# Performance work log

Hardware: AMD Instinct MI355X
Metric: run time of the kernel (lower is better)

Reference implementation:

```python
import jax, jax.numpy as jnp
import numpy as np

B, N, T, S = 1, 16, 2048, 2048
G, I = 1, 2
M = N // G  # heads per group


def setup_inputs() -> dict:
    key = jax.random.key(0)
    ks = jax.random.split(key, 8)
    return {
        "inputs": jax.random.normal(ks[0], (B, N, T, S), dtype=jnp.float32),
        "qw1": jax.random.normal(ks[1], (B, T, G, I, M), dtype=jnp.float32) * 0.05,
        "qw2": jax.random.normal(ks[2], (B, T, G, I, M), dtype=jnp.float32) * 0.05,
        "kw1": jax.random.normal(ks[3], (B, S, G, I, M), dtype=jnp.float32) * 0.05,
        "kw2": jax.random.normal(ks[4], (B, S, G, I, M), dtype=jnp.float32) * 0.05,
        "qdd": jax.random.normal(ks[5], (B, T, G, M), dtype=jnp.float32) * 0.05,
        "kdd": jax.random.normal(ks[6], (B, S, G, M), dtype=jnp.float32) * 0.05,
        "w": jax.random.normal(ks[7], (G, M, M), dtype=jnp.float32) * 0.02,
    }


def reference(inputs, qw1, qw2, kw1, kw2, qdd, kdd, w):
    b, n, t, s = inputs.shape
    g, m = w.shape[0], w.shape[1]
    x = inputs.reshape(b, g, m, t, s)  # BGMTS
    # static cross-head mixing (w + identity)
    wi = w + jnp.eye(m, dtype=w.dtype)
    ret = jnp.einsum('BGMTS,GMN->BGNTS', x, wi)
    # dynamic low-rank mixing, query-side (per T position); the original loops
    # over the I axis — summing over I is mathematically identical.
    hq = jnp.einsum('BGMTS,BTGIM->BGITS', x, qw1)
    ret = ret + jnp.einsum('BGITS,BTGIM->BGMTS', hq, qw2)
    # dynamic low-rank mixing, key-side (per S position)
    hk = jnp.einsum('BGMTS,BSGIM->BGITS', x, kw1)
    ret = ret + jnp.einsum('BGITS,BSGIM->BGMTS', hk, kw2)
    # dynamic diagonal terms
    ret = ret + jnp.einsum('BGMTS,BTGM->BGMTS', x, qdd)
    ret = ret + jnp.einsum('BGMTS,BSGM->BGMTS', x, kdd)
    return ret.reshape(b, n, t, s)
```

## Files before the change

kernel.cpp:

```cpp
#include <hip/hip_runtime.h>


#define TDIM 2048
#define SDIM 2048
#define TT 8
#define SBLK 256

typedef float vf4 __attribute__((ext_vector_type(4)));

__global__ void chp_prep(const float* __restrict__ kw1, const float* __restrict__ kw2,
                         const float* __restrict__ kdd,
                         float* __restrict__ kt1, float* __restrict__ kt2,
                         float* __restrict__ kddt) {
  int tid = blockIdx.x * blockDim.x + threadIdx.x;
  if (tid < 65536) {
    int im = tid >> 11, s = tid & 2047;
    kt1[tid] = kw1[s * 32 + im];
  } else if (tid < 131072) {
    int v = tid - 65536;
    int im = v >> 11, s = v & 2047;
    kt2[v] = kw2[s * 32 + im];
  } else if (tid < 163840) {
    int v = tid - 131072;
    int n = v >> 11, s = v & 2047;
    kddt[v] = kdd[s * 16 + n];
  }
}

__device__ __forceinline__ vf4 ld4(const float* p) {
  return *reinterpret_cast<const vf4*>(p);
}
__device__ __forceinline__ void fma4(vf4& d, const vf4& a, const vf4& b) {
  d.x = fmaf(a.x, b.x, d.x); d.y = fmaf(a.y, b.y, d.y);
  d.z = fmaf(a.z, b.z, d.z); d.w = fmaf(a.w, b.w, d.w);
}
__device__ __forceinline__ void fma4s(vf4& d, const vf4& a, float b) {
  d.x = fmaf(a.x, b, d.x); d.y = fmaf(a.y, b, d.y);
  d.z = fmaf(a.z, b, d.z); d.w = fmaf(a.w, b, d.w);
}

template <bool KT>
__global__ __launch_bounds__(256, 3) void chp_main(
    const float* __restrict__ in, const float* __restrict__ w,
    const float* __restrict__ qw1, const float* __restrict__ qw2,
    const float* __restrict__ qdd, const float* __restrict__ kw1,
    const float* __restrict__ kw2, const float* __restrict__ kdd,
    const float* __restrict__ kt1, const float* __restrict__ kt2,
    const float* __restrict__ kddt, float* __restrict__ out) {
  __shared__ vf4 x_lds[2][16][65];
  __shared__ float wq_lds[2][256];

  const int tid = threadIdx.x;
  const int j = tid & 3;
  const int qg = tid >> 2;
  const int s0 = blockIdx.x * SBLK + qg * 4;
  const int t0 = blockIdx.y * TT;

  vf4 kt1v[2][4], kt2v[2][4], kdv[4];
  if constexpr (KT) {
#pragma unroll
    for (int i = 0; i < 2; ++i)
#pragma unroll
      for (int k = 0; k < 4; ++k) {
        kt1v[i][k] = ld4(kt1 + (size_t)(i * 16 + 4 * j + k) * SDIM + s0);
        kt2v[i][k] = ld4(kt2 + (size_t)(i * 16 + 4 * j + k) * SDIM + s0);
      }
#pragma unroll
    for (int k = 0; k < 4; ++k) kdv[k] = ld4(kddt + (size_t)(4 * j + k) * SDIM + s0);
  } else {
#pragma unroll
    for (int i = 0; i < 2; ++i)
#pragma unroll
      for (int k = 0; k < 4; ++k)
#pragma unroll
        for (int c = 0; c < 4; ++c) {
          kt1v[i][k][c] = kw1[(size_t)(s0 + c) * 32 + i * 16 + 4 * j + k];
          kt2v[i][k][c] = kw2[(size_t)(s0 + c) * 32 + i * 16 + 4 * j + k];
        }
#pragma unroll
    for (int k = 0; k < 4; ++k)
#pragma unroll
      for (int c = 0; c < 4; ++c) kdv[k][c] = kdd[(size_t)(s0 + c) * 16 + 4 * j + k];
  }

  const int bm = tid >> 4, bn = tid & 15;
  const float wbase = w[bm * 16 + bn];

  vf4 xp[4];
#pragma unroll
  for (int k = 0; k < 4; ++k)
    xp[k] = ld4(in + ((size_t)(4 * j + k) * TDIM + t0) * SDIM + s0);
  float q1a = qw1[t0 * 32 + bm], q1b = qw1[t0 * 32 + 16 + bm];
  float q2a = qw2[t0 * 32 + bn], q2b = qw2[t0 * 32 + 16 + bn];
  float qd = qdd[t0 * 16 + bn];

#pragma unroll
  for (int k = 0; k < 4; ++k) x_lds[0][4 * j + k][qg] = xp[k];
  {
    float v = fmaf(q1a, q2a, wbase);
    v = fmaf(q1b, q2b, v);
    if (bm == bn) v += 1.0f + qd;
    wq_lds[0][tid] = v;
  }
  {
    const int t1 = t0 + 1;
#pragma unroll
    for (int k = 0; k < 4; ++k)
      xp[k] = ld4(in + ((size_t)(4 * j + k) * TDIM + t1) * SDIM + s0);
    q1a = qw1[t1 * 32 + bm]; q1b = qw1[t1 * 32 + 16 + bm];
    q2a = qw2[t1 * 32 + bn]; q2b = qw2[t1 * 32 + 16 + bn];
    qd = qdd[t1 * 16 + bn];
  }
  __syncthreads();

  int cur = 0;
  for (int tt = 0; tt < TT; ++tt) {
    const int t = t0 + tt;
    const int nxt = cur ^ 1;

    vf4 acc[4];
    vf4 p0 = (vf4){0.f, 0.f, 0.f, 0.f}, p1 = p0;
#pragma unroll
    for (int r = 0; r < 4; ++r) acc[r] = (vf4){0.f, 0.f, 0.f, 0.f};

#pragma unroll
    for (int m = 0; m < 16; ++m) {
      const vf4 xm = x_lds[cur][m][qg];
      const vf4 wr = *reinterpret_cast<const vf4*>(&wq_lds[cur][m * 16 + 4 * j]);
      fma4s(acc[0], xm, wr.x);
      fma4s(acc[1], xm, wr.y);
      fma4s(acc[2], xm, wr.z);
      fma4s(acc[3], xm, wr.w);
      if ((m >> 2) == j) {
        const int k = m & 3;
        fma4(p0, xm, kt1v[0][k]);
        fma4(p1, xm, kt1v[1][k]);
        fma4(acc[k], xm, kdv[k]);
      }
    }
#pragma unroll
    for (int mask = 1; mask <= 2; mask <<= 1) {
      p0.x += __shfl_xor(p0.x, mask); p0.y += __shfl_xor(p0.y, mask);
      p0.z += __shfl_xor(p0.z, mask); p0.w += __shfl_xor(p0.w, mask);
      p1.x += __shfl_xor(p1.x, mask); p1.y += __shfl_xor(p1.y, mask);
      p1.z += __shfl_xor(p1.z, mask); p1.w += __shfl_xor(p1.w, mask);
    }
#pragma unroll
    for (int r = 0; r < 4; ++r) {
      fma4(acc[r], p0, kt2v[0][r]);
      fma4(acc[r], p1, kt2v[1][r]);
      *reinterpret_cast<vf4*>(out + ((size_t)(4 * j + r) * TDIM + t) * SDIM + s0) =
          acc[r];
    }

    if (tt + 1 < TT) {
#pragma unroll
      for (int k = 0; k < 4; ++k) x_lds[nxt][4 * j + k][qg] = xp[k];
      float v = fmaf(q1a, q2a, wbase);
      v = fmaf(q1b, q2b, v);
      if (bm == bn) v += 1.0f + qd;
      wq_lds[nxt][tid] = v;
      if (tt + 2 < TT) {
        const int tp = t + 2;
#pragma unroll
        for (int k = 0; k < 4; ++k)
          xp[k] = ld4(in + ((size_t)(4 * j + k) * TDIM + tp) * SDIM + s0);
        q1a = qw1[tp * 32 + bm]; q1b = qw1[tp * 32 + 16 + bm];
        q2a = qw2[tp * 32 + bn]; q2b = qw2[tp * 32 + 16 + bn];
        qd = qdd[tp * 16 + bn];
      }
    }
    __syncthreads();
    cur = nxt;
  }
}

extern "C" void kernel_launch(void* const* d_in, const int* in_sizes, int n_in,
                              void* d_out, int out_size, void* d_ws, size_t ws_size,
                              hipStream_t stream) {
  const float* in = (const float*)d_in[0];
  const float* qw1 = (const float*)d_in[1];
  const float* qw2 = (const float*)d_in[2];
  const float* kw1 = (const float*)d_in[3];
  const float* kw2 = (const float*)d_in[4];
  const float* qdd = (const float*)d_in[5];
  const float* kdd = (const float*)d_in[6];
  const float* w = (const float*)d_in[7];
  float* out = (float*)d_out;
  float* ws = (float*)d_ws;

  const bool useKT = (ws_size >= 163840ull * sizeof(float));
  float* kt1 = ws;
  float* kt2 = ws + 65536;
  float* kddt = ws + 131072;

  dim3 grid(SDIM / SBLK, TDIM / TT);
  if (useKT) {
    hipLaunchKernelGGL(chp_prep, dim3(640), dim3(256), 0, stream, kw1, kw2, kdd, kt1,
                       kt2, kddt);
    hipLaunchKernelGGL((chp_main<true>), grid, dim3(256), 0, stream, in, w, qw1, qw2,
                       qdd, kw1, kw2, kdd, kt1, kt2, kddt, out);
  } else {
    hipLaunchKernelGGL((chp_main<false>), grid, dim3(256), 0, stream, in, w, qw1, qw2,
                       qdd, kw1, kw2, kdd, nullptr, nullptr, nullptr, out);
  }
}
```

Before: 158.7 us.

## Make LDS staging wave-local to eliminate block-wide barriers

Each 64-lane wavefront now owns its own 64-column slice of the S block and its own LDS buffers for the x tile and the per-t mixing matrix. Every wave computes the full 16x16 mixing matrix redundantly using vector loads, instead of the block sharing one. All __syncthreads calls are removed, and the next-step staging is moved before the shuffle reduction and stores. This is meant to remove barrier stalls and let waves drift independently to overlap memory traffic. The cost is redundant mixing-matrix work per wave and reliance on intra-wave ordering for LDS reuse without double buffering.

```diff
diff --git a/kernel.cpp b/kernel.cpp
--- a/kernel.cpp
+++ b/kernel.cpp
@@ -47,14 +47,18 @@
     const float* __restrict__ kw2, const float* __restrict__ kdd,
     const float* __restrict__ kt1, const float* __restrict__ kt2,
     const float* __restrict__ kddt, float* __restrict__ out) {
-  __shared__ vf4 x_lds[2][16][65];
-  __shared__ float wq_lds[2][256];
+  __shared__ vf4 x_lds[4][16][16];
+  __shared__ float wq_lds[4][256];
 
   const int tid = threadIdx.x;
-  const int j = tid & 3;
-  const int qg = tid >> 2;
-  const int s0 = blockIdx.x * SBLK + qg * 4;
+  const int wv = tid >> 6;
+  const int lane = tid & 63;
+  const int j = lane & 3;
+  const int qg = lane >> 2;
+  const int s0 = blockIdx.x * SBLK + wv * 64 + qg * 4;
   const int t0 = blockIdx.y * TT;
+  const int bm = qg;
+  const int bn4 = j * 4;
 
   vf4 kt1v[2][4], kt2v[2][4], kdv[4];
   if constexpr (KT) {
@@ -82,41 +86,45 @@
 #pragma unroll
       for (int c = 0; c < 4; ++c) kdv[k][c] = kdd[(size_t)(s0 + c) * 16 + 4 * j + k];
   }
-
-  const int bm = tid >> 4, bn = tid & 15;
-  const float wbase = w[bm * 16 + bn];
+  const vf4 wrow = ld4(w + bm * 16 + bn4);
 
   vf4 xp[4];
-#pragma unroll
-  for (int k = 0; k < 4; ++k)
-    xp[k] = ld4(in + ((size_t)(4 * j + k) * TDIM + t0) * SDIM + s0);
-  float q1a = qw1[t0 * 32 + bm], q1b = qw1[t0 * 32 + 16 + bm];
-  float q2a = qw2[t0 * 32 + bn], q2b = qw2[t0 * 32 + 16 + bn];
-  float qd = qdd[t0 * 16 + bn];
-
-#pragma unroll
-  for (int k = 0; k < 4; ++k) x_lds[0][4 * j + k][qg] = xp[k];
-  {
-    float v = fmaf(q1a, q2a, wbase);
-    v = fmaf(q1b, q2b, v);
-    if (bm == bn) v += 1.0f + qd;
-    wq_lds[0][tid] = v;
-  }
-  {
-    const int t1 = t0 + 1;
+  float q1a, q1b, qdq;
+  vf4 q2a, q2b;
+
+  auto prefetch = [&](int t) {
 #pragma unroll
     for (int k = 0; k < 4; ++k)
-      xp[k] = ld4(in + ((size_t)(4 * j + k) * TDIM + t1) * SDIM + s0);
-    q1a = qw1[t1 * 32 + bm]; q1b = qw1[t1 * 32 + 16 + bm];
-    q2a = qw2[t1 * 32 + bn]; q2b = qw2[t1 * 32 + 16 + bn];
-    qd = qdd[t1 * 16 + bn];
-  }
-  __syncthreads();
-
-  int cur = 0;
+      xp[k] = ld4(in + ((size_t)(4 * j + k) * TDIM + t) * SDIM + s0);
+    q1a = qw1[t * 32 + bm];
+    q1b = qw1[t * 32 + 16 + bm];
+    q2a = ld4(qw2 + t * 32 + bn4);
+    q2b = ld4(qw2 + t * 32 + 16 + bn4);
+    qdq = qdd[t * 16 + bm];
+  };
+  auto stage = [&]() {
+#pragma unroll
+    for (int k = 0; k < 4; ++k) x_lds[wv][4 * j + k][qg] = xp[k];
+    vf4 wqv;
+    wqv.x = fmaf(q1a, q2a.x, fmaf(q1b, q2b.x, wrow.x));
+    wqv.y = fmaf(q1a, q2a.y, fmaf(q1b, q2b.y, wrow.y));
+    wqv.z = fmaf(q1a, q2a.z, fmaf(q1b, q2b.z, wrow.z));
+    wqv.w = fmaf(q1a, q2a.w, fmaf(q1b, q2b.w, wrow.w));
+    const float dg = 1.0f + qdq;
+    wqv.x += (bm == bn4 + 0) ? dg : 0.0f;
+    wqv.y += (bm == bn4 + 1) ? dg : 0.0f;
+    wqv.z += (bm == bn4 + 2) ? dg : 0.0f;
+    wqv.w += (bm == bn4 + 3) ? dg : 0.0f;
+    *reinterpret_cast<vf4*>(&wq_lds[wv][lane * 4]) = wqv;
+  };
+
+  prefetch(t0);
+  stage();
+  prefetch(t0 + 1);
+
+#pragma unroll
   for (int tt = 0; tt < TT; ++tt) {
     const int t = t0 + tt;
-    const int nxt = cur ^ 1;
 
     vf4 acc[4];
     vf4 p0 = (vf4){0.f, 0.f, 0.f, 0.f}, p1 = p0;
@@ -125,8 +133,8 @@
 
 #pragma unroll
     for (int m = 0; m < 16; ++m) {
-      const vf4 xm = x_lds[cur][m][qg];
-      const vf4 wr = *reinterpret_cast<const vf4*>(&wq_lds[cur][m * 16 + 4 * j]);
+      const vf4 xm = x_lds[wv][m][qg];
+      const vf4 wr = *reinterpret_cast<const vf4*>(&wq_lds[wv][m * 16 + 4 * j]);
       fma4s(acc[0], xm, wr.x);
       fma4s(acc[1], xm, wr.y);
       fma4s(acc[2], xm, wr.z);
@@ -138,6 +146,10 @@
         fma4(acc[k], xm, kdv[k]);
       }
     }
+
+    if (tt + 1 < TT) stage();
+    if (tt + 2 < TT) prefetch(t + 2);
+
 #pragma unroll
     for (int mask = 1; mask <= 2; mask <<= 1) {
       p0.x += __shfl_xor(p0.x, mask); p0.y += __shfl_xor(p0.y, mask);
@@ -145,6 +157,7 @@
       p1.x += __shfl_xor(p1.x, mask); p1.y += __shfl_xor(p1.y, mask);
       p1.z += __shfl_xor(p1.z, mask); p1.w += __shfl_xor(p1.w, mask);
     }
+
 #pragma unroll
     for (int r = 0; r < 4; ++r) {
       fma4(acc[r], p0, kt2v[0][r]);
@@ -152,26 +165,6 @@
       *reinterpret_cast<vf4*>(out + ((size_t)(4 * j + r) * TDIM + t) * SDIM + s0) =
           acc[r];
     }
-
-    if (tt + 1 < TT) {
-#pragma unroll
-      for (int k = 0; k < 4; ++k) x_lds[nxt][4 * j + k][qg] = xp[k];
-      float v = fmaf(q1a, q2a, wbase);
-      v = fmaf(q1b, q2b, v);
-      if (bm == bn) v += 1.0f + qd;
-      wq_lds[nxt][tid] = v;
-      if (tt + 2 < TT) {
-        const int tp = t + 2;
-#pragma unroll
-        for (int k = 0; k < 4; ++k)
-          xp[k] = ld4(in + ((size_t)(4 * j + k) * TDIM + tp) * SDIM + s0);
-        q1a = qw1[tp * 32 + bm]; q1b = qw1[tp * 32 + 16 + bm];
-        q2a = qw2[tp * 32 + bn]; q2b = qw2[tp * 32 + 16 + bn];
-        qd = qdd[tp * 16 + bn];
-      }
-    }
-    __syncthreads();
-    cur = nxt;
   }
 }
 
```

Result: slower. 169.4 us (+6.7%).
